# Kernel optimization log

Measured on AMD Instinct MI355X. Metric: run time of the kernel, lower is better.

The kernel has to match this reference:

```python
import jax, jax.numpy as jnp
import numpy as np

B, T, C, H = 2, 2048, 1024, 16
HD = C // H  # head size = 64
EPS = 1e-5


def setup_inputs() -> dict:
    key = jax.random.key(0)
    ks = jax.random.split(key, 16)
    s = 0.02
    return {
        "x": jax.random.normal(ks[0], (B, T, C), jnp.float32),
        # per-head q/k/v projections, stacked: [H, C, HD]
        "Wq": jax.random.normal(ks[1], (H, C, HD), jnp.float32) * s,
        "Wk": jax.random.normal(ks[2], (H, C, HD), jnp.float32) * s,
        "Wv": jax.random.normal(ks[3], (H, C, HD), jnp.float32) * s,
        "Wproj": jax.random.normal(ks[4], (C, C), jnp.float32) * s,
        "bproj": jnp.zeros((C,), jnp.float32),
        "W1": jax.random.normal(ks[5], (C, 4 * C), jnp.float32) * s,
        "b1": jnp.zeros((4 * C,), jnp.float32),
        "W2": jax.random.normal(ks[6], (4 * C, C), jnp.float32) * s,
        "b2": jnp.zeros((C,), jnp.float32),
        "g1": jnp.ones((C,), jnp.float32),
        "be1": jnp.zeros((C,), jnp.float32),
        "g2": jnp.ones((C,), jnp.float32),
        "be2": jnp.zeros((C,), jnp.float32),
    }


def _layernorm(x, g, b):
    mu = jnp.mean(x, axis=-1, keepdims=True)
    var = jnp.mean(jnp.square(x - mu), axis=-1, keepdims=True)
    return (x - mu) * jax.lax.rsqrt(var + EPS) * g + b


def _block(x, Wq, Wk, Wv, Wproj, bproj, W1, b1, W2, b2, g1, be1, g2, be2):
    Bx, Tx, Cx = x.shape
    h = _layernorm(x, g1, be1)
    q = jnp.einsum("btc,hcd->bhtd", h, Wq)
    k = jnp.einsum("btc,hcd->bhtd", h, Wk)
    v = jnp.einsum("btc,hcd->bhtd", h, Wv)
    scores = jnp.einsum("bhtd,bhsd->bhts", q, k) * (HD ** -0.5)  # [B,H,T,T]
    causal = jnp.tril(jnp.ones((Tx, Tx), bool))
    scores = jnp.where(causal, scores, -jnp.inf)
    w = jax.nn.softmax(scores, axis=-1)
    o = jnp.einsum("bhts,bhsd->bhtd", w, v)
    o = o.transpose(0, 2, 1, 3).reshape(Bx, Tx, Cx)  # concat heads
    x = x + o @ Wproj + bproj
    h2 = _layernorm(x, g2, be2)
    ff = jax.nn.relu(h2 @ W1 + b1) @ W2 + b2
    return x + ff


def reference(x, Wq, Wk, Wv, Wproj, bproj, W1, b1, W2, b2, g1, be1, g2, be2):
    return _block(x, Wq, Wk, Wv, Wproj, bproj, W1, b1, W2, b2, g1, be1, g2, be2)
```

## Files before the change

kernel.cpp:

```cpp
#include <hip/hip_runtime.h>
#include <stdint.h>


typedef unsigned short u16;
typedef unsigned int u32;
typedef __attribute__((ext_vector_type(4))) float f32x4;
typedef __attribute__((ext_vector_type(8))) short s16x8;

__device__ __forceinline__ u16 f2bf(float f) {
  u32 u = __builtin_bit_cast(u32, f);
  u += 0x7fffu + ((u >> 16) & 1u);
  return (u16)(u >> 16);
}
__device__ __forceinline__ s16x8 ld_s16x8_a8(const u16* p) {
  union { uint2 d[2]; s16x8 v; } u;
  u.d[0] = *(const uint2*)p;
  u.d[1] = *(const uint2*)(p + 4);
  return u.v;
}
__device__ __forceinline__ void gload16(const u16* g, u16* lds_base) {
  __builtin_amdgcn_global_load_lds(
      (const __attribute__((address_space(1))) void*)g,
      (__attribute__((address_space(3))) void*)lds_base, 16, 0, 0);
}

__global__ __launch_bounds__(256) void transpose_f32_bf16(
    const float* __restrict__ src, u16* __restrict__ dst,
    int Ccols, long srcZ, long dstZ, int dstStride) {
  __shared__ float t[64][65];
  const float* s = src + (size_t)blockIdx.z * srcZ;
  u16* d = dst + (size_t)blockIdx.z * dstZ;
  const int r0 = blockIdx.y * 64, c0 = blockIdx.x * 64;
  const int tr = threadIdx.x >> 4, tc4 = (threadIdx.x & 15) * 4;
#pragma unroll
  for (int p = 0; p < 4; ++p) {
    int r = p * 16 + tr;
    float4 v = *(const float4*)(s + (size_t)(r0 + r) * Ccols + c0 + tc4);
    t[r][tc4 + 0] = v.x; t[r][tc4 + 1] = v.y;
    t[r][tc4 + 2] = v.z; t[r][tc4 + 3] = v.w;
  }
  __syncthreads();
#pragma unroll
  for (int p = 0; p < 4; ++p) {
    int c = p * 16 + tr;
    uint2 pk;
    pk.x = (u32)f2bf(t[tc4 + 0][c]) | ((u32)f2bf(t[tc4 + 1][c]) << 16);
    pk.y = (u32)f2bf(t[tc4 + 2][c]) | ((u32)f2bf(t[tc4 + 3][c]) << 16);
    *(uint2*)(d + (size_t)(c0 + c) * dstStride + r0 + tc4) = pk;
  }
}

__global__ __launch_bounds__(256) void ln_kernel(
    const float* __restrict__ x, const float* __restrict__ g,
    const float* __restrict__ be, u16* __restrict__ out) {
  const int row = blockIdx.x, tid = threadIdx.x;
  const float* xr = x + (size_t)row * 1024;
  float4 v = *(const float4*)(xr + tid * 4);
  float s = v.x + v.y + v.z + v.w;
  float q = v.x * v.x + v.y * v.y + v.z * v.z + v.w * v.w;
#pragma unroll
  for (int off = 32; off > 0; off >>= 1) {
    s += __shfl_down(s, off);
    q += __shfl_down(q, off);
  }
  __shared__ float red[8];
  const int wid = tid >> 6, lane = tid & 63;
  if (lane == 0) { red[wid] = s; red[wid + 4] = q; }
  __syncthreads();
  s = red[0] + red[1] + red[2] + red[3];
  q = red[4] + red[5] + red[6] + red[7];
  const float mu = s * (1.f / 1024.f);
  const float var = q * (1.f / 1024.f) - mu * mu;
  const float rs = rsqrtf(var + 1e-5f);
  float4 gv = *(const float4*)(g + tid * 4);
  float4 bv = *(const float4*)(be + tid * 4);
  float o0 = (v.x - mu) * rs * gv.x + bv.x;
  float o1 = (v.y - mu) * rs * gv.y + bv.y;
  float o2 = (v.z - mu) * rs * gv.z + bv.z;
  float o3 = (v.w - mu) * rs * gv.w + bv.w;
  uint2 pk;
  pk.x = (u32)f2bf(o0) | ((u32)f2bf(o1) << 16);
  pk.y = (u32)f2bf(o2) | ((u32)f2bf(o3) << 16);
  *(uint2*)(out + (size_t)row * 1024 + tid * 4) = pk;
}

template <int EPI, int BM>
__global__ __launch_bounds__(256) void gemm_kernel(
    const u16* __restrict__ A, const u16* __restrict__ BT,
    const float* __restrict__ bias, const float* __restrict__ resid,
    void* __restrict__ out, int M, int N, int K) {
  __shared__ u16 sA[BM][64];
  __shared__ u16 sB[128][64];
  const int tid = threadIdx.x;
  const int m0 = blockIdx.y * BM, n0 = blockIdx.x * 128;
  const int wid = tid >> 6, lane = tid & 63;
  const int wr = (wid >> 1) * (BM / 2), wc = (wid & 1) * 64;
  const int l15 = lane & 15, g = lane >> 4;
  constexpr int MR = BM / 32;
  f32x4 acc[MR][4] = {};
  const int lr = lane >> 3;
  const int cswz = ((lane & 7) * 8) ^ (lr << 3);

  for (int k0 = 0; k0 < K; k0 += 64) {
    __syncthreads();
#pragma unroll
    for (int p = 0; p < MR; ++p) {
      const int row = (p * 4 + wid) * 8 + lr;
      gload16(A + (size_t)(m0 + row) * K + k0 + cswz, &sA[(p * 4 + wid) * 8][0]);
    }
#pragma unroll
    for (int p = 0; p < 4; ++p) {
      const int row = (p * 4 + wid) * 8 + lr;
      gload16(BT + (size_t)(n0 + row) * K + k0 + cswz, &sB[(p * 4 + wid) * 8][0]);
    }
    __syncthreads();
#pragma unroll
    for (int kk = 0; kk < 64; kk += 32) {
      s16x8 af[MR], bf[4];
#pragma unroll
      for (int m = 0; m < MR; ++m) {
        const int R = wr + m * 16 + l15;
        af[m] = *(const s16x8*)(&sA[R][(kk + g * 8) ^ ((R & 7) << 3)]);
      }
#pragma unroll
      for (int n = 0; n < 4; ++n) {
        const int R = wc + n * 16 + l15;
        bf[n] = *(const s16x8*)(&sB[R][(kk + g * 8) ^ ((R & 7) << 3)]);
      }
#pragma unroll
      for (int m = 0; m < MR; ++m)
#pragma unroll
        for (int n = 0; n < 4; ++n)
          acc[m][n] = __builtin_amdgcn_mfma_f32_16x16x32_bf16(af[m], bf[n], acc[m][n], 0, 0, 0);
    }
  }

#pragma unroll
  for (int m = 0; m < MR; ++m) {
#pragma unroll
    for (int n = 0; n < 4; ++n) {
      const int col = n0 + wc + n * 16 + l15;
      float bv = 0.f;
      if (EPI >= 1) bv = bias[col];
#pragma unroll
      for (int i = 0; i < 4; ++i) {
        const int row = m0 + wr + m * 16 + g * 4 + i;
        float v = acc[m][n][i];
        if (EPI >= 1) v += bv;
        if (EPI == 1) v = fmaxf(v, 0.f);
        if (EPI == 2) {
          v += resid[(size_t)row * N + col];
          ((float*)out)[(size_t)row * N + col] = v;
        } else {
          ((u16*)out)[(size_t)row * N + col] = f2bf(v);
        }
      }
    }
  }
}

template <int EPI>
__global__ __launch_bounds__(512, 2) void gemm256_kernel(
    const u16* __restrict__ A, const u16* __restrict__ BT,
    const float* __restrict__ bias, const float* __restrict__ resid,
    void* __restrict__ out, int M, int N, int K) {
  __shared__ u16 lds[2][2][256][64];
  const int tid = threadIdx.x;
  const int wid = tid >> 6, lane = tid & 63;
  const int m0 = blockIdx.y * 256, n0 = blockIdx.x * 256;
  const int wr = (wid >> 2) * 128;
  const int wc = (wid & 3) * 64;
  const int l15 = lane & 15, g = lane >> 4;
  const int lr = lane >> 3;
  const int cswz = ((lane & 7) * 8) ^ (lr << 3);
  const int swz = (l15 & 7) << 3;
  const u16* Abase = A + (size_t)m0 * K;
  const u16* Bbase = BT + (size_t)n0 * K;
  const int nkt = K >> 6;

  f32x4 acc[8][4] = {};
  s16x8 bf[4][2];

  auto issue_half = [&](const u16* Xbase, int xi, int t, int hf) {
    const int b = t & 1;
    const int r0 = hf * 128 + wid * 8;
    gload16(Xbase + (size_t)(r0 + lr) * K + t * 64 + cswz, &lds[b][xi][r0][0]);
    gload16(Xbase + (size_t)(r0 + 64 + lr) * K + t * 64 + cswz, &lds[b][xi][r0 + 64][0]);
  };

  issue_half(Abase, 0, 0, 0);
  issue_half(Abase, 0, 0, 1);
  issue_half(Bbase, 1, 0, 0);
  issue_half(Bbase, 1, 0, 1);
  asm volatile("s_waitcnt vmcnt(0)" ::: "memory");
  __builtin_amdgcn_s_barrier();

  for (int i = 0; i < nkt; i += 2) {
#pragma unroll
    for (int p = 0; p < 4; ++p) {
      s16x8 af[2][2];
#pragma unroll
      for (int q = 0; q < 2; ++q) {
        const int R = wr + (2 * p + q) * 16 + l15;
#pragma unroll
        for (int h = 0; h < 2; ++h)
          af[q][h] = *(const s16x8*)(&lds[0][0][R][(h * 32 + g * 8) ^ swz]);
      }
      if (p == 0) {
#pragma unroll
        for (int n = 0; n < 4; ++n) {
          const int R = wc + n * 16 + l15;
#pragma unroll
          for (int h = 0; h < 2; ++h)
            bf[n][h] = *(const s16x8*)(&lds[0][1][R][(h * 32 + g * 8) ^ swz]);
        }
      }
      if (i + 1 < nkt) {
        if (p == 0) issue_half(Abase, 0, i + 1, 0);
        else if (p == 1) issue_half(Abase, 0, i + 1, 1);
        else if (p == 2) issue_half(Bbase, 1, i + 1, 0);
        else issue_half(Bbase, 1, i + 1, 1);
      }
      __builtin_amdgcn_s_barrier();
      asm volatile("s_waitcnt lgkmcnt(0)" ::: "memory");
      __builtin_amdgcn_sched_barrier(0);
      __builtin_amdgcn_s_setprio(1);
#pragma unroll
      for (int q = 0; q < 2; ++q)
#pragma unroll
        for (int n = 0; n < 4; ++n) {
          acc[2 * p + q][n] = __builtin_amdgcn_mfma_f32_16x16x32_bf16(af[q][0], bf[n][0], acc[2 * p + q][n], 0, 0, 0);
          acc[2 * p + q][n] = __builtin_amdgcn_mfma_f32_16x16x32_bf16(af[q][1], bf[n][1], acc[2 * p + q][n], 0, 0, 0);
        }
      __builtin_amdgcn_s_setprio(0);
      if (p == 3)
        asm volatile("s_waitcnt vmcnt(0)" ::: "memory");
      __builtin_amdgcn_s_barrier();
    }
    if (i + 1 < nkt) {
#pragma unroll
      for (int p = 0; p < 4; ++p) {
        s16x8 af[2][2];
#pragma unroll
        for (int q = 0; q < 2; ++q) {
          const int R = wr + (2 * p + q) * 16 + l15;
#pragma unroll
          for (int h = 0; h < 2; ++h)
            af[q][h] = *(const s16x8*)(&lds[1][0][R][(h * 32 + g * 8) ^ swz]);
        }
        if (p == 0) {
#pragma unroll
          for (int n = 0; n < 4; ++n) {
            const int R = wc + n * 16 + l15;
#pragma unroll
            for (int h = 0; h < 2; ++h)
              bf[n][h] = *(const s16x8*)(&lds[1][1][R][(h * 32 + g * 8) ^ swz]);
          }
        }
        if (i + 2 < nkt) {
          if (p == 0) issue_half(Abase, 0, i + 2, 0);
          else if (p == 1) issue_half(Abase, 0, i + 2, 1);
          else if (p == 2) issue_half(Bbase, 1, i + 2, 0);
          else issue_half(Bbase, 1, i + 2, 1);
        }
        __builtin_amdgcn_s_barrier();
        asm volatile("s_waitcnt lgkmcnt(0)" ::: "memory");
        __builtin_amdgcn_sched_barrier(0);
        __builtin_amdgcn_s_setprio(1);
#pragma unroll
        for (int q = 0; q < 2; ++q)
#pragma unroll
          for (int n = 0; n < 4; ++n) {
            acc[2 * p + q][n] = __builtin_amdgcn_mfma_f32_16x16x32_bf16(af[q][0], bf[n][0], acc[2 * p + q][n], 0, 0, 0);
            acc[2 * p + q][n] = __builtin_amdgcn_mfma_f32_16x16x32_bf16(af[q][1], bf[n][1], acc[2 * p + q][n], 0, 0, 0);
          }
        __builtin_amdgcn_s_setprio(0);
        if (p == 3)
          asm volatile("s_waitcnt vmcnt(0)" ::: "memory");
        __builtin_amdgcn_s_barrier();
      }
    }
  }

#pragma unroll
  for (int mi = 0; mi < 8; ++mi)
#pragma unroll
    for (int n = 0; n < 4; ++n) {
      const int col = n0 + wc + n * 16 + l15;
      float bv = (EPI >= 1) ? bias[col] : 0.f;
#pragma unroll
      for (int ii = 0; ii < 4; ++ii) {
        const int row = m0 + wr + mi * 16 + g * 4 + ii;
        float v = acc[mi][n][ii];
        if (EPI >= 1) v += bv;
        if (EPI == 1) v = fmaxf(v, 0.f);
        ((u16*)out)[(size_t)row * N + col] = f2bf(v);
      }
    }
}

__global__ __launch_bounds__(256) void attn_mfma_kernel(
    const u16* __restrict__ qkv, u16* __restrict__ o) {
  __shared__ u16 sK[64][72];
  __shared__ u16 sVt[64][68];
  __shared__ u16 sP[4][16][72];
  const int tid = threadIdx.x;
  const int b = blockIdx.y >> 4, h = blockIdx.y & 15;
  const int w = tid >> 6, lane = tid & 63;
  const int l15 = lane & 15, g = lane >> 4;
  const float c = 0.125f * 1.4426950408889634f;
  const int ks_r = tid >> 2, ks_c = (tid & 3) * 16;
  const int vs_s = tid & 63, vs_d = (tid >> 6) * 8;
  const u16* kbase = qkv + (size_t)(b * 2048) * 3072 + 1024 + h * 64;
  const u16* vbase = kbase + 1024;

#pragma unroll 1
  for (int pass = 0; pass < 2; ++pass) {
    const int qb = pass == 0 ? (31 - (int)blockIdx.x) : (int)blockIdx.x;

    const size_t qrow = (size_t)(b * 2048 + qb * 64 + w * 16 + l15);
    s16x8 qf0 = *(const s16x8*)(qkv + qrow * 3072 + h * 64 + g * 8);
    s16x8 qf1 = *(const s16x8*)(qkv + qrow * 3072 + h * 64 + 32 + g * 8);

    f32x4 oacc[4] = {};
    float mrow[4] = {-1e30f, -1e30f, -1e30f, -1e30f};
    float lrow[4] = {0.f, 0.f, 0.f, 0.f};

    const int nt = qb + 1;
    uint4 kr0, kr1, vr0, vr1;
    {
      const u16* kp = kbase + (size_t)(ks_r)*3072 + ks_c;
      kr0 = *(const uint4*)kp; kr1 = *(const uint4*)(kp + 8);
      const u16* vp = vbase + (size_t)(vs_s)*3072 + vs_d;
      vr0 = *(const uint4*)vp; vr1 = *(const uint4*)(vp + 32);
    }
    for (int t = 0; t < nt; ++t) {
      __syncthreads();
      *(uint4*)(&sK[ks_r][ks_c]) = kr0;
      *(uint4*)(&sK[ks_r][ks_c + 8]) = kr1;
      {
        union { uint4 q4; u16 e[8]; } va, vb;
        va.q4 = vr0; vb.q4 = vr1;
#pragma unroll
        for (int j = 0; j < 8; ++j) sVt[vs_d + j][vs_s] = va.e[j];
#pragma unroll
        for (int j = 0; j < 8; ++j) sVt[vs_d + 32 + j][vs_s] = vb.e[j];
      }
      __syncthreads();
      if (t + 1 < nt) {
        const u16* kp = kbase + (size_t)((t + 1) * 64 + ks_r) * 3072 + ks_c;
        kr0 = *(const uint4*)kp; kr1 = *(const uint4*)(kp + 8);
        const u16* vp = vbase + (size_t)((t + 1) * 64 + vs_s) * 3072 + vs_d;
        vr0 = *(const uint4*)vp; vr1 = *(const uint4*)(vp + 32);
      }

      f32x4 st[4];
#pragma unroll
      for (int n = 0; n < 4; ++n) {
        s16x8 k0 = *(const s16x8*)(&sK[n * 16 + l15][g * 8]);
        s16x8 k1 = *(const s16x8*)(&sK[n * 16 + l15][32 + g * 8]);
        f32x4 a = {};
        a = __builtin_amdgcn_mfma_f32_16x16x32_bf16(qf0, k0, a, 0, 0, 0);
        a = __builtin_amdgcn_mfma_f32_16x16x32_bf16(qf1, k1, a, 0, 0, 0);
        st[n] = a;
      }
      if (t == qb) {
#pragma unroll
        for (int n = 0; n < 4; ++n)
#pragma unroll
          for (int i = 0; i < 4; ++i) {
            const int srel = n * 16 + l15, qrel = w * 16 + 4 * g + i;
            if (srel > qrel) st[n][i] = -1e30f;
          }
      }
      float pm[4];
#pragma unroll
      for (int i = 0; i < 4; ++i)
        pm[i] = fmaxf(fmaxf(st[0][i], st[1][i]), fmaxf(st[2][i], st[3][i]));
#pragma unroll
      for (int msk = 1; msk < 16; msk <<= 1)
#pragma unroll
        for (int i = 0; i < 4; ++i) pm[i] = fmaxf(pm[i], __shfl_xor(pm[i], msk));
      float corr[4];
#pragma unroll
      for (int i = 0; i < 4; ++i) {
        const float mnew = fmaxf(mrow[i], pm[i]);
        corr[i] = exp2f((mrow[i] - mnew) * c);
        mrow[i] = mnew;
        lrow[i] *= corr[i];
      }
#pragma unroll
      for (int dt = 0; dt < 4; ++dt)
#pragma unroll
        for (int i = 0; i < 4; ++i) oacc[dt][i] *= corr[i];
      float p[4][4];
#pragma unroll
      for (int n = 0; n < 4; ++n)
#pragma unroll
        for (int i = 0; i < 4; ++i) p[n][i] = exp2f((st[n][i] - mrow[i]) * c);
#pragma unroll
      for (int i = 0; i < 4; ++i)
        lrow[i] += (p[0][i] + p[1][i]) + (p[2][i] + p[3][i]);
#pragma unroll
      for (int n = 0; n < 4; ++n)
#pragma unroll
        for (int i = 0; i < 4; ++i)
          sP[w][4 * g + i][n * 16 + l15] = f2bf(p[n][i]);
      s16x8 pf0 = *(const s16x8*)(&sP[w][l15][g * 8]);
      s16x8 pf1 = *(const s16x8*)(&sP[w][l15][32 + g * 8]);
#pragma unroll
      for (int dt = 0; dt < 4; ++dt) {
        s16x8 vf0 = ld_s16x8_a8(&sVt[dt * 16 + l15][g * 8]);
        s16x8 vf1 = ld_s16x8_a8(&sVt[dt * 16 + l15][32 + g * 8]);
        oacc[dt] = __builtin_amdgcn_mfma_f32_16x16x32_bf16(pf0, vf0, oacc[dt], 0, 0, 0);
        oacc[dt] = __builtin_amdgcn_mfma_f32_16x16x32_bf16(pf1, vf1, oacc[dt], 0, 0, 0);
      }
    }

#pragma unroll
    for (int msk = 1; msk < 16; msk <<= 1)
#pragma unroll
      for (int i = 0; i < 4; ++i) lrow[i] += __shfl_xor(lrow[i], msk);
    float inv[4];
#pragma unroll
    for (int i = 0; i < 4; ++i) inv[i] = 1.f / lrow[i];
#pragma unroll
    for (int dt = 0; dt < 4; ++dt)
#pragma unroll
      for (int i = 0; i < 4; ++i) {
        const size_t row = (size_t)(b * 2048 + qb * 64 + w * 16 + 4 * g + i);
        o[row * 1024 + h * 64 + dt * 16 + l15] = f2bf(oacc[dt][i] * inv[i]);
      }
  }
}

extern "C" void kernel_launch(void* const* d_in, const int* in_sizes, int n_in,
                              void* d_out, int out_size, void* d_ws, size_t ws_size,
                              hipStream_t stream) {
  const float* x     = (const float*)d_in[0];
  const float* Wq    = (const float*)d_in[1];
  const float* Wk    = (const float*)d_in[2];
  const float* Wv    = (const float*)d_in[3];
  const float* Wproj = (const float*)d_in[4];
  const float* bproj = (const float*)d_in[5];
  const float* W1    = (const float*)d_in[6];
  const float* b1    = (const float*)d_in[7];
  const float* W2    = (const float*)d_in[8];
  const float* b2    = (const float*)d_in[9];
  const float* g1    = (const float*)d_in[10];
  const float* be1   = (const float*)d_in[11];
  const float* g2    = (const float*)d_in[12];
  const float* be2   = (const float*)d_in[13];
  float* out = (float*)d_out;

  u16* WqkvT  = (u16*)d_ws;
  u16* WprojT = WqkvT + (size_t)3072 * 1024;
  u16* W1T    = WprojT + (size_t)1024 * 1024;
  u16* W2T    = W1T + (size_t)4096 * 1024;
  u16* hbuf   = W2T + (size_t)1024 * 4096;
  u16* qkv    = hbuf + (size_t)4096 * 1024;
  u16* obuf   = qkv + (size_t)4096 * 3072;
  float* x2   = (float*)(obuf + (size_t)4096 * 1024);
  u16* a1     = (u16*)(x2 + (size_t)4096 * 1024);

  transpose_f32_bf16<<<dim3(1, 16, 16), 256, 0, stream>>>(Wq, WqkvT,                      64, 65536, 65536, 1024);
  transpose_f32_bf16<<<dim3(1, 16, 16), 256, 0, stream>>>(Wk, WqkvT + (size_t)1024 * 1024, 64, 65536, 65536, 1024);
  transpose_f32_bf16<<<dim3(1, 16, 16), 256, 0, stream>>>(Wv, WqkvT + (size_t)2048 * 1024, 64, 65536, 65536, 1024);
  transpose_f32_bf16<<<dim3(16, 16, 1), 256, 0, stream>>>(Wproj, WprojT, 1024, 0, 0, 1024);
  transpose_f32_bf16<<<dim3(64, 16, 1), 256, 0, stream>>>(W1, W1T, 4096, 0, 0, 1024);
  transpose_f32_bf16<<<dim3(16, 64, 1), 256, 0, stream>>>(W2, W2T, 1024, 0, 0, 4096);

  ln_kernel<<<4096, 256, 0, stream>>>(x, g1, be1, hbuf);
  gemm_kernel<0, 128><<<dim3(24, 32), 256, 0, stream>>>(hbuf, WqkvT, nullptr, nullptr, qkv, 4096, 3072, 1024);
  attn_mfma_kernel<<<dim3(16, 32), 256, 0, stream>>>(qkv, obuf);
  gemm_kernel<2, 64><<<dim3(8, 64), 256, 0, stream>>>(obuf, WprojT, bproj, x, x2, 4096, 1024, 1024);
  ln_kernel<<<4096, 256, 0, stream>>>(x2, g2, be2, hbuf);
  gemm256_kernel<1><<<dim3(16, 16), 512, 0, stream>>>(hbuf, W1T, b1, nullptr, a1, 4096, 4096, 1024);
  gemm_kernel<2, 64><<<dim3(8, 64), 256, 0, stream>>>(a1, W2T, b2, x2, out, 4096, 1024, 4096);
}
```

Before: 272.3 us.

## Add 128x128 pipelined GEMM for N=1024 projections and lazy softmax rescale

Adds a new 512-thread 128x128-tile GEMM with double-buffered direct-to-LDS loads, swizzled LDS layout and interleaved prefetch, and uses it for the attention output projection and the second FFN GEMM in place of the 64-row tile kernel. Separately, the attention kernel now rescales the running max and output accumulator only when some row's new max exceeds the old one by a threshold, which skips most exp and multiply work per tile. The threshold-based rescale lets exponentials exceed 1 by a bounded factor, which carries some numerical risk. The grid for the replaced GEMMs halves to 256 blocks, which could lower occupancy on the device.

```diff
diff --git a/kernel.cpp b/kernel.cpp
--- a/kernel.cpp
+++ b/kernel.cpp
@@ -299,6 +299,144 @@
     }
 }
 
+template <int EPI>
+__global__ __launch_bounds__(512, 2) void gemm128_kernel(
+    const u16* __restrict__ A, const u16* __restrict__ BT,
+    const float* __restrict__ bias, const float* __restrict__ resid,
+    void* __restrict__ out, int M, int N, int K) {
+  __shared__ u16 lds[2][2][128][64];
+  const int tid = threadIdx.x;
+  const int wid = tid >> 6, lane = tid & 63;
+  const int m0 = blockIdx.y * 128, n0 = blockIdx.x * 128;
+  const int wr = (wid >> 2) * 64;
+  const int wc = (wid & 3) * 32;
+  const int l15 = lane & 15, g = lane >> 4;
+  const int lr = lane >> 3;
+  const int cswz = ((lane & 7) * 8) ^ (lr << 3);
+  const int swz = (l15 & 7) << 3;
+  const u16* Abase = A + (size_t)m0 * K;
+  const u16* Bbase = BT + (size_t)n0 * K;
+  const int nkt = K >> 6;
+
+  f32x4 acc[4][2] = {};
+  s16x8 bf[2][2];
+
+  auto issue_half = [&](const u16* Xbase, int xi, int t, int hf) {
+    const int b = t & 1;
+    const int r0 = hf * 64 + wid * 8;
+    gload16(Xbase + (size_t)(r0 + lr) * K + t * 64 + cswz, &lds[b][xi][r0][0]);
+  };
+
+  issue_half(Abase, 0, 0, 0); issue_half(Abase, 0, 0, 1);
+  issue_half(Bbase, 1, 0, 0); issue_half(Bbase, 1, 0, 1);
+  asm volatile("s_waitcnt vmcnt(0)" ::: "memory");
+  __builtin_amdgcn_s_barrier();
+
+  for (int i = 0; i < nkt; i += 2) {
+#pragma unroll
+    for (int p = 0; p < 2; ++p) {
+      s16x8 af[2][2];
+#pragma unroll
+      for (int q = 0; q < 2; ++q) {
+        const int R = wr + (2 * p + q) * 16 + l15;
+#pragma unroll
+        for (int h = 0; h < 2; ++h)
+          af[q][h] = *(const s16x8*)(&lds[0][0][R][(h * 32 + g * 8) ^ swz]);
+      }
+      if (p == 0) {
+#pragma unroll
+        for (int n = 0; n < 2; ++n) {
+          const int R = wc + n * 16 + l15;
+#pragma unroll
+          for (int h = 0; h < 2; ++h)
+            bf[n][h] = *(const s16x8*)(&lds[0][1][R][(h * 32 + g * 8) ^ swz]);
+        }
+      }
+      if (i + 1 < nkt) {
+        if (p == 0) { issue_half(Abase, 0, i + 1, 0); issue_half(Abase, 0, i + 1, 1); }
+        else        { issue_half(Bbase, 1, i + 1, 0); issue_half(Bbase, 1, i + 1, 1); }
+      }
+      __builtin_amdgcn_s_barrier();
+      asm volatile("s_waitcnt lgkmcnt(0)" ::: "memory");
+      __builtin_amdgcn_sched_barrier(0);
+      __builtin_amdgcn_s_setprio(1);
+#pragma unroll
+      for (int q = 0; q < 2; ++q)
+#pragma unroll
+        for (int n = 0; n < 2; ++n) {
+          acc[2 * p + q][n] = __builtin_amdgcn_mfma_f32_16x16x32_bf16(af[q][0], bf[n][0], acc[2 * p + q][n], 0, 0, 0);
+          acc[2 * p + q][n] = __builtin_amdgcn_mfma_f32_16x16x32_bf16(af[q][1], bf[n][1], acc[2 * p + q][n], 0, 0, 0);
+        }
+      __builtin_amdgcn_s_setprio(0);
+      if (p == 1)
+        asm volatile("s_waitcnt vmcnt(0)" ::: "memory");
+      __builtin_amdgcn_s_barrier();
+    }
+    if (i + 1 < nkt) {
+#pragma unroll
+      for (int p = 0; p < 2; ++p) {
+        s16x8 af[2][2];
+#pragma unroll
+        for (int q = 0; q < 2; ++q) {
+          const int R = wr + (2 * p + q) * 16 + l15;
+#pragma unroll
+          for (int h = 0; h < 2; ++h)
+            af[q][h] = *(const s16x8*)(&lds[1][0][R][(h * 32 + g * 8) ^ swz]);
+        }
+        if (p == 0) {
+#pragma unroll
+          for (int n = 0; n < 2; ++n) {
+            const int R = wc + n * 16 + l15;
+#pragma unroll
+            for (int h = 0; h < 2; ++h)
+              bf[n][h] = *(const s16x8*)(&lds[1][1][R][(h * 32 + g * 8) ^ swz]);
+          }
+        }
+        if (i + 2 < nkt) {
+          if (p == 0) { issue_half(Abase, 0, i + 2, 0); issue_half(Abase, 0, i + 2, 1); }
+          else        { issue_half(Bbase, 1, i + 2, 0); issue_half(Bbase, 1, i + 2, 1); }
+        }
+        __builtin_amdgcn_s_barrier();
+        asm volatile("s_waitcnt lgkmcnt(0)" ::: "memory");
+        __builtin_amdgcn_sched_barrier(0);
+        __builtin_amdgcn_s_setprio(1);
+#pragma unroll
+        for (int q = 0; q < 2; ++q)
+#pragma unroll
+          for (int n = 0; n < 2; ++n) {
+            acc[2 * p + q][n] = __builtin_amdgcn_mfma_f32_16x16x32_bf16(af[q][0], bf[n][0], acc[2 * p + q][n], 0, 0, 0);
+            acc[2 * p + q][n] = __builtin_amdgcn_mfma_f32_16x16x32_bf16(af[q][1], bf[n][1], acc[2 * p + q][n], 0, 0, 0);
+          }
+        __builtin_amdgcn_s_setprio(0);
+        if (p == 1)
+          asm volatile("s_waitcnt vmcnt(0)" ::: "memory");
+        __builtin_amdgcn_s_barrier();
+      }
+    }
+  }
+
+#pragma unroll
+  for (int mi = 0; mi < 4; ++mi)
+#pragma unroll
+    for (int n = 0; n < 2; ++n) {
+      const int col = n0 + wc + n * 16 + l15;
+      float bv = (EPI >= 1) ? bias[col] : 0.f;
+#pragma unroll
+      for (int ii = 0; ii < 4; ++ii) {
+        const int row = m0 + wr + mi * 16 + g * 4 + ii;
+        float v = acc[mi][n][ii];
+        if (EPI >= 1) v += bv;
+        if (EPI == 1) v = fmaxf(v, 0.f);
+        if (EPI == 2) {
+          v += resid[(size_t)row * N + col];
+          ((float*)out)[(size_t)row * N + col] = v;
+        } else {
+          ((u16*)out)[(size_t)row * N + col] = f2bf(v);
+        }
+      }
+    }
+}
+
 __global__ __launch_bounds__(256) void attn_mfma_kernel(
     const u16* __restrict__ qkv, u16* __restrict__ o) {
   __shared__ u16 sK[64][72];
@@ -381,18 +519,20 @@
       for (int msk = 1; msk < 16; msk <<= 1)
 #pragma unroll
         for (int i = 0; i < 4; ++i) pm[i] = fmaxf(pm[i], __shfl_xor(pm[i], msk));
-      float corr[4];
-#pragma unroll
-      for (int i = 0; i < 4; ++i) {
-        const float mnew = fmaxf(mrow[i], pm[i]);
-        corr[i] = exp2f((mrow[i] - mnew) * c);
-        mrow[i] = mnew;
-        lrow[i] *= corr[i];
-      }
-#pragma unroll
-      for (int dt = 0; dt < 4; ++dt)
-#pragma unroll
-        for (int i = 0; i < 4; ++i) oacc[dt][i] *= corr[i];
+      bool need = false;
+#pragma unroll
+      for (int i = 0; i < 4; ++i) need = need || (pm[i] > mrow[i] + 12.f);
+      if (__any(need)) {
+#pragma unroll
+        for (int i = 0; i < 4; ++i) {
+          const float mnew = fmaxf(mrow[i], pm[i]);
+          const float corr = exp2f((mrow[i] - mnew) * c);
+          mrow[i] = mnew;
+          lrow[i] *= corr;
+#pragma unroll
+          for (int dt = 0; dt < 4; ++dt) oacc[dt][i] *= corr;
+        }
+      }
       float p[4][4];
 #pragma unroll
       for (int n = 0; n < 4; ++n)
@@ -473,8 +613,8 @@
   ln_kernel<<<4096, 256, 0, stream>>>(x, g1, be1, hbuf);
   gemm_kernel<0, 128><<<dim3(24, 32), 256, 0, stream>>>(hbuf, WqkvT, nullptr, nullptr, qkv, 4096, 3072, 1024);
   attn_mfma_kernel<<<dim3(16, 32), 256, 0, stream>>>(qkv, obuf);
-  gemm_kernel<2, 64><<<dim3(8, 64), 256, 0, stream>>>(obuf, WprojT, bproj, x, x2, 4096, 1024, 1024);
+  gemm128_kernel<2><<<dim3(8, 32), 512, 0, stream>>>(obuf, WprojT, bproj, x, x2, 4096, 1024, 1024);
   ln_kernel<<<4096, 256, 0, stream>>>(x2, g2, be2, hbuf);
   gemm256_kernel<1><<<dim3(16, 16), 512, 0, stream>>>(hbuf, W1T, b1, nullptr, a1, 4096, 4096, 1024);
-  gemm_kernel<2, 64><<<dim3(8, 64), 256, 0, stream>>>(a1, W2T, b2, x2, out, 4096, 1024, 4096);
-}
+  gemm128_kernel<2><<<dim3(8, 32), 512, 0, stream>>>(a1, W2T, b2, x2, out, 4096, 1024, 4096);
+}
```

Result: no change. 277.2 us (+1.8%).
